# Kernel tuning notes

Hardware: AMD Instinct MI355X
Metric: run time of the kernel (lower is better)

## Reference

```python
import jax, jax.numpy as jnp
import numpy as np

N_NODES = 50000
N_EDGES = 800000
N_GRAPHS = 256
F_IN, HID, EMB = 128, 256, 128
N_GROUPS, N_FAM = 16, 128


def setup_inputs() -> dict:
    key = jax.random.key(0)
    ks = jax.random.split(key, 12)
    x = jax.random.normal(ks[0], (N_NODES, F_IN), dtype=jnp.float32)
    edge_index = jax.random.randint(ks[1], (2, N_EDGES), 0, N_NODES, dtype=jnp.int64)
    batch = jnp.sort(jax.random.randint(ks[2], (N_NODES,), 0, N_GRAPHS, dtype=jnp.int64))
    def lin(k, fi, fo):
        s = 1.0 / np.sqrt(fi)
        return jax.random.uniform(k, (fi, fo), minval=-s, maxval=s, dtype=jnp.float32)
    W1 = lin(ks[3], F_IN, HID); b1 = jnp.zeros((HID,), jnp.float32)
    W2 = lin(ks[4], HID, EMB); b2 = jnp.zeros((EMB,), jnp.float32)
    Wg = lin(ks[5], EMB, N_GROUPS); bg = jnp.zeros((N_GROUPS,), jnp.float32)
    s = 1.0 / np.sqrt(EMB)
    Wf = jax.random.uniform(ks[6], (N_GROUPS, EMB, N_FAM), minval=-s, maxval=s, dtype=jnp.float32)
    bf = jnp.zeros((N_GROUPS, N_FAM), jnp.float32)
    return {"x": x, "edge_index": edge_index, "batch": batch,
            "W1": W1, "b1": b1, "W2": W2, "b2": b2,
            "Wg": Wg, "bg": bg, "Wf": Wf, "bf": bf}


def _gcn_conv(h, src, dst, coef, W, b, n):
    # h: [N, Fin]; src/dst: [E'] (self-loops included); coef: [E'] sym-norm
    hw = h @ W                                    # [N, Fout]
    msg = hw[src] * coef[:, None]                 # gather + scale, [E', Fout]
    out = jax.ops.segment_sum(msg, dst, num_segments=n)  # scatter-add
    return out + b


def reference(x, edge_index, batch, W1, b1, W2, b2, Wg, bg, Wf, bf):
    n = x.shape[0]
    loops = jnp.arange(n, dtype=edge_index.dtype)
    src = jnp.concatenate([edge_index[0], loops])
    dst = jnp.concatenate([edge_index[1], loops])
    # symmetric GCN normalization (deg >= 1 thanks to self-loops)
    deg = jax.ops.segment_sum(jnp.ones_like(dst, dtype=x.dtype), dst, num_segments=n)
    dinv = jax.lax.rsqrt(deg)
    coef = dinv[src] * dinv[dst]

    h1 = jax.nn.relu(_gcn_conv(x, src, dst, coef, W1, b1, n))  # dropout = identity (eval)
    h2 = _gcn_conv(h1, src, dst, coef, W2, b2, n)

    # global mean pool over graphs
    sums = jax.ops.segment_sum(h2, batch, num_segments=N_GRAPHS)
    cnts = jax.ops.segment_sum(jnp.ones((n,), x.dtype), batch, num_segments=N_GRAPHS)
    embeddings = sums / jnp.maximum(cnts, 1.0)[:, None]        # [G, EMB]

    group_logits = embeddings @ Wg + bg                        # [G, n_groups]
    pred_groups = jnp.argmax(group_logits, axis=1)             # routing
    # per-graph routed family classifier (dense equivalent of the dict outputs)
    family_logits = jnp.einsum('gd,gdf->gf', embeddings, Wf[pred_groups]) + bf[pred_groups]
    return embeddings, group_logits, family_logits
```

## Files before the change

kernel.cpp:

```cpp
#include <hip/hip_runtime.h>
#include <hip/hip_fp16.h>
#include <cstddef>
#include <cstdint>

static constexpr int NN   = 50000;
static constexpr int NE   = 800000;
static constexpr int NG   = 256;
static constexpr int FIN  = 128;
static constexpr int HID  = 256;
static constexpr int EMB  = 128;
static constexpr int NGRP = 16;
static constexpr int NFAM = 128;
static constexpr int NETOT = NE + NN;

static constexpr int SCAN_B  = 256;
static constexpr int SCAN_CH = (NN + SCAN_B - 1) / SCAN_B;

static constexpr int NSLICE  = 8;
static constexpr int SLICE_W = (NN + NSLICE - 1) / NSLICE;
static constexpr int BUILD_RANKS = 64;

using bf16x8 = __attribute__((ext_vector_type(8))) short;
using f32x4  = __attribute__((ext_vector_type(4))) float;

__device__ __forceinline__ unsigned short f2bf(float f) {
    uint32_t u = __float_as_uint(f);
    u += 0x7FFFu + ((u >> 16) & 1u);
    return (unsigned short)(u >> 16);
}
__device__ __forceinline__ float bf2f(unsigned short u) {
    return __uint_as_float((uint32_t)u << 16);
}
__device__ __forceinline__ uint32_t pack_sw(int s, float w) {
    return (uint32_t)s | ((uint32_t)__half_as_ushort(__float2half(w)) << 16);
}
__device__ __forceinline__ void unpack_sw(uint32_t v, int& s, float& w) {
    s = (int)(v & 0xFFFFu);
    w = __half2float(__ushort_as_half((unsigned short)(v >> 16)));
}


__global__ void k_count(const int* __restrict__ edst, int* __restrict__ degi, int e) {
    int i = blockIdx.x * blockDim.x + threadIdx.x;
    if (i < e) atomicAdd(degi + edst[i], 1);
}

__global__ void k_prep(const int* __restrict__ degi, const int* __restrict__ batch,
                       float* __restrict__ dinv, int* __restrict__ gstart,
                       float* __restrict__ emb_acc, int n, int G) {
    int i = blockIdx.x * blockDim.x + threadIdx.x;
    if (i < NG * EMB) emb_acc[i] = 0.f;
    if (i >= n) return;
    dinv[i] = rsqrtf((float)(degi[i] + 1));
    int b  = batch[i];
    int pb = (i == 0) ? -1 : batch[i - 1];
    for (int g = pb + 1; g <= b; ++g) gstart[g] = i;
    if (i == n - 1) {
        for (int g = b + 1; g <= G; ++g) gstart[g] = n;
    }
}

__global__ void k_xconv(const float* __restrict__ x, const float* __restrict__ dinv,
                        unsigned short* __restrict__ xs) {
    int t = blockIdx.x * blockDim.x + threadIdx.x;
    size_t i = (size_t)t * 8;
    float dv = dinv[t >> 4];
    float4 a = *(const float4*)(x + i);
    float4 b = *(const float4*)(x + i + 4);
    uint4 o;
    o.x = (uint32_t)f2bf(dv * a.x) | ((uint32_t)f2bf(dv * a.y) << 16);
    o.y = (uint32_t)f2bf(dv * a.z) | ((uint32_t)f2bf(dv * a.w) << 16);
    o.z = (uint32_t)f2bf(dv * b.x) | ((uint32_t)f2bf(dv * b.y) << 16);
    o.w = (uint32_t)f2bf(dv * b.z) | ((uint32_t)f2bf(dv * b.w) << 16);
    *(uint4*)(xs + i) = o;
}

__global__ void k_wconv(const float* __restrict__ W1, const float* __restrict__ W2,
                        unsigned short* __restrict__ W1t, unsigned short* __restrict__ W2t) {
    int t = blockIdx.x * blockDim.x + threadIdx.x;
    if (t < HID * FIN) {
        int nidx = t >> 7, k = t & 127;
        W1t[t] = f2bf(W1[(size_t)k * HID + nidx]);
    } else {
        int u = t - HID * FIN;
        int nidx = u >> 8, k = u & 255;
        W2t[u] = f2bf(W2[(size_t)k * EMB + nidx]);
    }
}


__global__ __launch_bounds__(256) void k_scanA(const int* __restrict__ degi,
                                               int* __restrict__ row_ptr,
                                               int* __restrict__ bsum, int n) {
    __shared__ int sh[256];
    const int b = blockIdx.x, t = threadIdx.x;
    const int idx = b * SCAN_CH + t;
    int v = 0;
    if (t < SCAN_CH && idx < n) v = degi[idx] + 1;
    sh[t] = v;
    __syncthreads();
    for (int off = 1; off < 256; off <<= 1) {
        int y = (t >= off) ? sh[t - off] : 0;
        __syncthreads();
        if (t >= off) sh[t] += y;
        __syncthreads();
    }
    if (t < SCAN_CH && idx < n) row_ptr[idx] = sh[t] - v;
    if (t == 255) bsum[b] = sh[255];
}

__global__ __launch_bounds__(256) void k_scanB(const int* __restrict__ bsum,
                                               const int* __restrict__ gstart,
                                               float* __restrict__ rcnt,
                                               int* __restrict__ row_ptr,
                                               int* __restrict__ cursor, int n) {
    __shared__ int sh[SCAN_B];
    const int b = blockIdx.x, t = threadIdx.x;
    sh[t] = bsum[t];
    __syncthreads();
    for (int off = 1; off < SCAN_B; off <<= 1) {
        int y = (t >= off) ? sh[t - off] : 0;
        __syncthreads();
        if (t >= off) sh[t] += y;
        __syncthreads();
    }
    const int boff = (b == 0) ? 0 : sh[b - 1];
    const int idx  = b * SCAN_CH + t;
    if (t < SCAN_CH && idx < n) {
        row_ptr[idx] += boff;
        cursor[idx] = 1;
    }
    if (b == 0 && t == 0) row_ptr[n] = sh[SCAN_B - 1];
    if (b == 0 && t < NG) {
        int c = gstart[t + 1] - gstart[t];
        rcnt[t] = 1.0f / (float)max(c, 1);
    }
}


__global__ __launch_bounds__(256) void k_build(
        const int* __restrict__ esrc, const int* __restrict__ edst,
        const int* __restrict__ batch, const float* __restrict__ dinv,
        const float* __restrict__ rcnt, const int* __restrict__ row_ptr,
        int* __restrict__ cursor, uint32_t* __restrict__ eP, int n, int e) {
    const int slice = blockIdx.x & 7;
    const int rank  = blockIdx.x >> 3;
    const int lo = slice * SLICE_W;
    const int hi = min(lo + SLICE_W, n);
    for (int i = lo + rank * 256 + (int)threadIdx.x; i < hi; i += BUILD_RANKS * 256) {
        eP[row_ptr[i]] = pack_sw(i, dinv[i] * rcnt[batch[i]]);
    }
    for (int j = rank * 256 + (int)threadIdx.x; j < e; j += BUILD_RANKS * 256) {
        int d = edst[j];
        if (d < lo || d >= hi) continue;
        int s = esrc[j];
        int p = atomicAdd(cursor + d, 1);
        eP[row_ptr[d] + p] = pack_sw(s, dinv[d] * rcnt[batch[d]]);
    }
}


__global__ __launch_bounds__(256) void k_agg(
        const unsigned short* __restrict__ xs, const int* __restrict__ row_ptr,
        const uint32_t* __restrict__ eP, const float* __restrict__ dinv,
        unsigned short* __restrict__ xa, int n) {
    int node = blockIdx.x * 4 + (threadIdx.x >> 6);
    if (node >= n) return;
    int lane = threadIdx.x & 63;
    int grp = lane >> 4, fl = lane & 15;
    float acc[8] = {};
    int beg = row_ptr[node], end = row_ptr[node + 1];
    for (int j = beg; j < end; j += 4) {
        int jj = j + grp;
        bool valid = jj < end;
        uint32_t ev = __builtin_nontemporal_load(eP + (valid ? jj : beg));
        int s = (int)(ev & 0xFFFFu);
        float m = valid ? 1.f : 0.f;
        bf16x8 v = *(const bf16x8*)(xs + ((size_t)s << 7) + fl * 8);
#pragma unroll
        for (int k = 0; k < 8; ++k)
            acc[k] += m * bf2f((unsigned short)v[k]);
    }
#pragma unroll
    for (int k = 0; k < 8; ++k) {
        acc[k] += __shfl_xor(acc[k], 16);
        acc[k] += __shfl_xor(acc[k], 32);
    }
    if (lane < 16) {
        float di = dinv[node];
        uint4 o;
        o.x = (uint32_t)f2bf(di * acc[0]) | ((uint32_t)f2bf(di * acc[1]) << 16);
        o.y = (uint32_t)f2bf(di * acc[2]) | ((uint32_t)f2bf(di * acc[3]) << 16);
        o.z = (uint32_t)f2bf(di * acc[4]) | ((uint32_t)f2bf(di * acc[5]) << 16);
        o.w = (uint32_t)f2bf(di * acc[6]) | ((uint32_t)f2bf(di * acc[7]) << 16);
        *(uint4*)(xa + ((size_t)node << 7) + fl * 8) = o;
    }
}


__global__ __launch_bounds__(256) void k_fgemm(
        const unsigned short* __restrict__ A,
        const unsigned short* __restrict__ W1t,
        const unsigned short* __restrict__ W2t,
        const float* __restrict__ b1, const float* __restrict__ dinv,
        unsigned short* __restrict__ H, int M) {
    __shared__ unsigned short h1s[64 * 256];
    const int m0 = blockIdx.x * 64;
    const int w  = threadIdx.x >> 6;
    const int l  = threadIdx.x & 63;
    const int lr = l & 15;
    const int lk = l >> 4;

    {
        f32x4 acc[4][4] = {};
        const int n0 = w * 64;
#pragma unroll
        for (int ks = 0; ks < 4; ++ks) {
            const int k0 = ks * 32 + lk * 8;
            bf16x8 bfr[4];
#pragma unroll
            for (int ni = 0; ni < 4; ++ni)
                bfr[ni] = *(const bf16x8*)(W1t + (size_t)(n0 + ni * 16 + lr) * FIN + k0);
#pragma unroll
            for (int mi = 0; mi < 4; ++mi) {
                int row = min(m0 + mi * 16 + lr, M - 1);
                bf16x8 afr = *(const bf16x8*)(A + ((size_t)row << 7) + k0);
#pragma unroll
                for (int ni = 0; ni < 4; ++ni)
                    acc[mi][ni] = __builtin_amdgcn_mfma_f32_16x16x32_bf16(
                        afr, bfr[ni], acc[mi][ni], 0, 0, 0);
            }
        }
#pragma unroll
        for (int ni = 0; ni < 4; ++ni) {
            int col = n0 + ni * 16 + lr;
            float bb = b1[col];
#pragma unroll
            for (int mi = 0; mi < 4; ++mi) {
#pragma unroll
                for (int r = 0; r < 4; ++r) {
                    int rl = mi * 16 + lk * 4 + r;
                    float dv = dinv[min(m0 + rl, M - 1)];
                    float v = fmaxf(acc[mi][ni][r] + bb, 0.f) * dv;
                    int byte = (rl * 512 + col * 2) ^ ((rl & 7) << 4);
                    *(unsigned short*)((char*)h1s + byte) = f2bf(v);
                }
            }
        }
    }
    __syncthreads();
    f32x4 acc2[4][2] = {};
    {
        const int n0 = w * 32;
#pragma unroll
        for (int ks = 0; ks < 8; ++ks) {
            const int k0 = ks * 32 + lk * 8;
            bf16x8 bfr[2];
#pragma unroll
            for (int ni = 0; ni < 2; ++ni)
                bfr[ni] = *(const bf16x8*)(W2t + (size_t)(n0 + ni * 16 + lr) * HID + k0);
#pragma unroll
            for (int mi = 0; mi < 4; ++mi) {
                int rl = mi * 16 + lr;
                int byte = (rl * 512 + k0 * 2) ^ ((rl & 7) << 4);
                bf16x8 afr = *(const bf16x8*)((const char*)h1s + byte);
#pragma unroll
                for (int ni = 0; ni < 2; ++ni)
                    acc2[mi][ni] = __builtin_amdgcn_mfma_f32_16x16x32_bf16(
                        afr, bfr[ni], acc2[mi][ni], 0, 0, 0);
            }
        }
    }
    __syncthreads();
    {
        const int n0 = w * 32;
#pragma unroll
        for (int ni = 0; ni < 2; ++ni) {
            int col = n0 + ni * 16 + lr;
#pragma unroll
            for (int mi = 0; mi < 4; ++mi)
#pragma unroll
                for (int r = 0; r < 4; ++r) {
                    int rl = mi * 16 + lk * 4 + r;
                    h1s[rl * EMB + col] = f2bf(acc2[mi][ni][r]);
                }
        }
    }
    __syncthreads();
    int nrows = min(64, M - m0);
    for (int c = threadIdx.x; c < nrows * 16; c += 256) {
        int rl = c >> 4, cc = c & 15;
        *(uint4*)(H + ((size_t)(m0 + rl) << 7) + cc * 8) =
            *(const uint4*)(h1s + rl * EMB + cc * 8);
    }
}


__global__ __launch_bounds__(256) void k_pool(
        const unsigned short* __restrict__ H, const int* __restrict__ row_ptr,
        const int* __restrict__ gstart, const uint32_t* __restrict__ eP,
        float* __restrict__ emb_acc) {
    __shared__ float red[4][EMB];
    const int g  = blockIdx.x >> 3;
    const int kb = blockIdx.x & 7;
    const int e0 = row_ptr[gstart[g]];
    const int e1 = row_ptr[gstart[g + 1]];
    const int len = e1 - e0;
    const int per = (len + 7) >> 3;
    const int s0  = e0 + kb * per;
    const int s1  = min(s0 + per, e1);
    const int lane = threadIdx.x & 63;
    const int wv   = threadIdx.x >> 6;
    const int grp = lane >> 4, fl = lane & 15;

    float acc[8] = {};
    for (int j = s0 + wv * 4; j < s1; j += 16) {
        int jj = j + grp;
        bool valid = jj < s1;
        uint32_t ev = __builtin_nontemporal_load(eP + (valid ? jj : s0));
        int s; float wgt;
        unpack_sw(ev, s, wgt);
        if (!valid) wgt = 0.f;
        bf16x8 v = *(const bf16x8*)(H + ((size_t)s << 7) + fl * 8);
#pragma unroll
        for (int k = 0; k < 8; ++k)
            acc[k] += wgt * bf2f((unsigned short)v[k]);
    }
#pragma unroll
    for (int k = 0; k < 8; ++k) {
        acc[k] += __shfl_xor(acc[k], 16);
        acc[k] += __shfl_xor(acc[k], 32);
    }
    if (lane < 16) {
#pragma unroll
        for (int k = 0; k < 8; ++k) red[wv][fl * 8 + k] = acc[k];
    }
    __syncthreads();
    int t = threadIdx.x;
    if (t < EMB) {
        float v = red[0][t] + red[1][t] + red[2][t] + red[3][t];
        if (v != 0.f) atomicAdd(&emb_acc[g * EMB + t], v);
    }
}


__global__ __launch_bounds__(128) void k_head(const float* __restrict__ emb_acc,
                                              const int* __restrict__ gstart,
                                              const float* __restrict__ b2,
                                              const float* __restrict__ Wg,
                                              const float* __restrict__ bg,
                                              const float* __restrict__ Wf,
                                              const float* __restrict__ bff,
                                              float* __restrict__ out_emb,
                                              float* __restrict__ out_gl,
                                              float* __restrict__ out_fl) {
    __shared__ float e[EMB];
    __shared__ float gl[NGRP];
    __shared__ int ps;
    int g = blockIdx.x, c = threadIdx.x;
    bool nonempty = gstart[g + 1] > gstart[g];
    float a = emb_acc[g * EMB + c] + (nonempty ? b2[c] : 0.f);
    e[c] = a;
    out_emb[(size_t)g * EMB + c] = a;
    __syncthreads();
    if (c < NGRP) {
        float s = bg[c];
        for (int d = 0; d < EMB; ++d) s += e[d] * Wg[d * NGRP + c];
        gl[c] = s;
        out_gl[g * NGRP + c] = s;
    }
    __syncthreads();
    if (c == 0) {
        int bi = 0;
        float bv = gl[0];
        for (int t2 = 1; t2 < NGRP; ++t2)
            if (gl[t2] > bv) { bv = gl[t2]; bi = t2; }
        ps = bi;
    }
    __syncthreads();
    int pr = ps;
    float s = bff[pr * NFAM + c];
    for (int d = 0; d < EMB; ++d) s += e[d] * Wf[((size_t)pr * EMB + d) * NFAM + c];
    out_fl[g * NFAM + c] = s;
}


extern "C" void kernel_launch(void* const* d_in, const int* in_sizes, int n_in,
                              void* d_out, int out_size, void* d_ws, size_t ws_size,
                              hipStream_t stream) {
    const float* x   = (const float*)d_in[0];
    const int*   ei  = (const int*)d_in[1];
    const int*   bat = (const int*)d_in[2];
    const float* W1  = (const float*)d_in[3];
    const float* b1  = (const float*)d_in[4];
    const float* W2  = (const float*)d_in[5];
    const float* b2  = (const float*)d_in[6];
    const float* Wg  = (const float*)d_in[7];
    const float* bg  = (const float*)d_in[8];
    const float* Wf  = (const float*)d_in[9];
    const float* bf  = (const float*)d_in[10];

    float* out     = (float*)d_out;
    float* out_emb = out;
    float* out_gl  = out + (size_t)NG * EMB;
    float* out_fl  = out_gl + (size_t)NG * NGRP;

    char* w = (char*)d_ws;
    auto alloc = [&](size_t bytes) {
        char* p = w;
        w += (bytes + 255) & ~(size_t)255;
        return p;
    };
    int*            degi    = (int*)alloc((size_t)NN * 4);
    float*          dinv    = (float*)alloc((size_t)NN * 4);
    int*            row_ptr = (int*)alloc((size_t)(NN + 1) * 4);
    int*            cursor  = (int*)alloc((size_t)NN * 4);
    int*            bsum    = (int*)alloc((size_t)SCAN_B * 4);
    uint32_t*       eP      = (uint32_t*)alloc((size_t)NETOT * 4);
    int*            gstart  = (int*)alloc((size_t)(NG + 1) * 4);
    float*          rcnt    = (float*)alloc((size_t)NG * 4);
    unsigned short* xs      = (unsigned short*)alloc((size_t)NN * FIN * 2);
    unsigned short* xa      = (unsigned short*)alloc((size_t)NN * FIN * 2);
    unsigned short* W1t     = (unsigned short*)alloc((size_t)HID * FIN * 2);
    unsigned short* W2t     = (unsigned short*)alloc((size_t)EMB * HID * 2);
    unsigned short* H       = (unsigned short*)alloc((size_t)NN * EMB * 2);
    float*          emb_acc = (float*)alloc((size_t)NG * EMB * 4);

    const int* esrc = ei;
    const int* edst = ei + NE;

    hipMemsetAsync(degi, 0, (size_t)NN * 4, stream);
    k_count<<<(NE + 255) / 256, 256, 0, stream>>>(edst, degi, NE);
    k_prep<<<(NG * HID + 255) / 256, 256, 0, stream>>>(degi, bat, dinv, gstart,
                                                       emb_acc, NN, NG);
    k_xconv<<<(NN * 16) / 256, 256, 0, stream>>>(x, dinv, xs);
    k_wconv<<<(HID * FIN + EMB * HID) / 256, 256, 0, stream>>>(W1, W2, W1t, W2t);
    k_scanA<<<SCAN_B, 256, 0, stream>>>(degi, row_ptr, bsum, NN);
    k_scanB<<<SCAN_B, 256, 0, stream>>>(bsum, gstart, rcnt, row_ptr, cursor, NN);
    k_build<<<NSLICE * BUILD_RANKS, 256, 0, stream>>>(esrc, edst, bat, dinv, rcnt,
                                                      row_ptr, cursor, eP, NN, NE);

    k_agg<<<(NN + 3) / 4, 256, 0, stream>>>(xs, row_ptr, eP, dinv, xa, NN);
    k_fgemm<<<(NN + 63) / 64, 256, 0, stream>>>(xa, W1t, W2t, b1, dinv, H, NN);

    k_pool<<<NG * 8, 256, 0, stream>>>(H, row_ptr, gstart, eP, emb_acc);

    k_head<<<NG, 128, 0, stream>>>(emb_acc, gstart, b2, Wg, bg, Wf, bf,
                                   out_emb, out_gl, out_fl);
}
```

Measured before the change: 223.4 us.

## Pack CSR cursor and edge weight into one 64-bit word for single-pass build

The CSR build no longer uses 8 destination slices, each of which rescanned all edges. It now runs one thread per edge and does a single 64-bit atomicAdd on a combined word that holds the write cursor and the precomputed half-precision weight. The scanB kernel initialises this combined word and writes the self-loop entries, and the rcnt computation moves into scanA. This removes the repeated edge reads and the per-edge dinv, batch and rcnt lookups, at the cost of 64-bit atomics scattered over 50k destinations without slice locality.

```diff
diff --git a/kernel.cpp b/kernel.cpp
--- a/kernel.cpp
+++ b/kernel.cpp
@@ -16,10 +16,6 @@
 static constexpr int SCAN_B  = 256;
 static constexpr int SCAN_CH = (NN + SCAN_B - 1) / SCAN_B;
 
-static constexpr int NSLICE  = 8;
-static constexpr int SLICE_W = (NN + NSLICE - 1) / NSLICE;
-static constexpr int BUILD_RANKS = 64;
-
 using bf16x8 = __attribute__((ext_vector_type(8))) short;
 using f32x4  = __attribute__((ext_vector_type(4))) float;
 
@@ -30,9 +26,6 @@
 }
 __device__ __forceinline__ float bf2f(unsigned short u) {
     return __uint_as_float((uint32_t)u << 16);
-}
-__device__ __forceinline__ uint32_t pack_sw(int s, float w) {
-    return (uint32_t)s | ((uint32_t)__half_as_ushort(__float2half(w)) << 16);
 }
 __device__ __forceinline__ void unpack_sw(uint32_t v, int& s, float& w) {
     s = (int)(v & 0xFFFFu);
@@ -90,10 +83,16 @@
 
 
 __global__ __launch_bounds__(256) void k_scanA(const int* __restrict__ degi,
+                                               const int* __restrict__ gstart,
+                                               float* __restrict__ rcnt,
                                                int* __restrict__ row_ptr,
                                                int* __restrict__ bsum, int n) {
+    const int b = blockIdx.x, t = threadIdx.x;
+    if (b == 0 && t < NG) {
+        int c = gstart[t + 1] - gstart[t];
+        rcnt[t] = 1.0f / (float)max(c, 1);
+    }
     __shared__ int sh[256];
-    const int b = blockIdx.x, t = threadIdx.x;
     const int idx = b * SCAN_CH + t;
     int v = 0;
     if (t < SCAN_CH && idx < n) v = degi[idx] + 1;
@@ -110,10 +109,12 @@
 }
 
 __global__ __launch_bounds__(256) void k_scanB(const int* __restrict__ bsum,
-                                               const int* __restrict__ gstart,
-                                               float* __restrict__ rcnt,
+                                               const int* __restrict__ batch,
+                                               const float* __restrict__ dinv,
+                                               const float* __restrict__ rcnt,
                                                int* __restrict__ row_ptr,
-                                               int* __restrict__ cursor, int n) {
+                                               unsigned long long* __restrict__ combo,
+                                               uint32_t* __restrict__ eP, int n) {
     __shared__ int sh[SCAN_B];
     const int b = blockIdx.x, t = threadIdx.x;
     sh[t] = bsum[t];
@@ -127,36 +128,28 @@
     const int boff = (b == 0) ? 0 : sh[b - 1];
     const int idx  = b * SCAN_CH + t;
     if (t < SCAN_CH && idx < n) {
-        row_ptr[idx] += boff;
-        cursor[idx] = 1;
+        int rp = row_ptr[idx] + boff;
+        row_ptr[idx] = rp;
+        unsigned short wh = __half_as_ushort(
+            __float2half(dinv[idx] * rcnt[batch[idx]]));
+        combo[idx] = ((unsigned long long)wh << 32) | (unsigned int)(rp + 1);
+        eP[rp] = (uint32_t)idx | ((uint32_t)wh << 16);
     }
     if (b == 0 && t == 0) row_ptr[n] = sh[SCAN_B - 1];
-    if (b == 0 && t < NG) {
-        int c = gstart[t + 1] - gstart[t];
-        rcnt[t] = 1.0f / (float)max(c, 1);
-    }
-}
-
-
-__global__ __launch_bounds__(256) void k_build(
-        const int* __restrict__ esrc, const int* __restrict__ edst,
-        const int* __restrict__ batch, const float* __restrict__ dinv,
-        const float* __restrict__ rcnt, const int* __restrict__ row_ptr,
-        int* __restrict__ cursor, uint32_t* __restrict__ eP, int n, int e) {
-    const int slice = blockIdx.x & 7;
-    const int rank  = blockIdx.x >> 3;
-    const int lo = slice * SLICE_W;
-    const int hi = min(lo + SLICE_W, n);
-    for (int i = lo + rank * 256 + (int)threadIdx.x; i < hi; i += BUILD_RANKS * 256) {
-        eP[row_ptr[i]] = pack_sw(i, dinv[i] * rcnt[batch[i]]);
-    }
-    for (int j = rank * 256 + (int)threadIdx.x; j < e; j += BUILD_RANKS * 256) {
-        int d = edst[j];
-        if (d < lo || d >= hi) continue;
-        int s = esrc[j];
-        int p = atomicAdd(cursor + d, 1);
-        eP[row_ptr[d] + p] = pack_sw(s, dinv[d] * rcnt[batch[d]]);
-    }
+}
+
+
+__global__ void k_build(const int* __restrict__ esrc, const int* __restrict__ edst,
+                        unsigned long long* __restrict__ combo,
+                        uint32_t* __restrict__ eP, int e) {
+    int j = blockIdx.x * blockDim.x + threadIdx.x;
+    if (j >= e) return;
+    int d = edst[j];
+    int s = esrc[j];
+    unsigned long long old = atomicAdd(combo + d, 1ull);
+    uint32_t slot = (uint32_t)old;
+    uint32_t wh   = (uint32_t)(old >> 32) & 0xFFFFu;
+    eP[slot] = (uint32_t)s | (wh << 16);
 }
 
 
@@ -411,20 +404,20 @@
         w += (bytes + 255) & ~(size_t)255;
         return p;
     };
-    int*            degi    = (int*)alloc((size_t)NN * 4);
-    float*          dinv    = (float*)alloc((size_t)NN * 4);
-    int*            row_ptr = (int*)alloc((size_t)(NN + 1) * 4);
-    int*            cursor  = (int*)alloc((size_t)NN * 4);
-    int*            bsum    = (int*)alloc((size_t)SCAN_B * 4);
-    uint32_t*       eP      = (uint32_t*)alloc((size_t)NETOT * 4);
-    int*            gstart  = (int*)alloc((size_t)(NG + 1) * 4);
-    float*          rcnt    = (float*)alloc((size_t)NG * 4);
-    unsigned short* xs      = (unsigned short*)alloc((size_t)NN * FIN * 2);
-    unsigned short* xa      = (unsigned short*)alloc((size_t)NN * FIN * 2);
-    unsigned short* W1t     = (unsigned short*)alloc((size_t)HID * FIN * 2);
-    unsigned short* W2t     = (unsigned short*)alloc((size_t)EMB * HID * 2);
-    unsigned short* H       = (unsigned short*)alloc((size_t)NN * EMB * 2);
-    float*          emb_acc = (float*)alloc((size_t)NG * EMB * 4);
+    int*                 degi    = (int*)alloc((size_t)NN * 4);
+    float*               dinv    = (float*)alloc((size_t)NN * 4);
+    int*                 row_ptr = (int*)alloc((size_t)(NN + 1) * 4);
+    unsigned long long*  combo   = (unsigned long long*)alloc((size_t)NN * 8);
+    int*                 bsum    = (int*)alloc((size_t)SCAN_B * 4);
+    uint32_t*            eP      = (uint32_t*)alloc((size_t)NETOT * 4);
+    int*                 gstart  = (int*)alloc((size_t)(NG + 1) * 4);
+    float*               rcnt    = (float*)alloc((size_t)NG * 4);
+    unsigned short*      xs      = (unsigned short*)alloc((size_t)NN * FIN * 2);
+    unsigned short*      xa      = (unsigned short*)alloc((size_t)NN * FIN * 2);
+    unsigned short*      W1t     = (unsigned short*)alloc((size_t)HID * FIN * 2);
+    unsigned short*      W2t     = (unsigned short*)alloc((size_t)EMB * HID * 2);
+    unsigned short*      H       = (unsigned short*)alloc((size_t)NN * EMB * 2);
+    float*               emb_acc = (float*)alloc((size_t)NG * EMB * 4);
 
     const int* esrc = ei;
     const int* edst = ei + NE;
@@ -435,10 +428,9 @@
                                                        emb_acc, NN, NG);
     k_xconv<<<(NN * 16) / 256, 256, 0, stream>>>(x, dinv, xs);
     k_wconv<<<(HID * FIN + EMB * HID) / 256, 256, 0, stream>>>(W1, W2, W1t, W2t);
-    k_scanA<<<SCAN_B, 256, 0, stream>>>(degi, row_ptr, bsum, NN);
-    k_scanB<<<SCAN_B, 256, 0, stream>>>(bsum, gstart, rcnt, row_ptr, cursor, NN);
-    k_build<<<NSLICE * BUILD_RANKS, 256, 0, stream>>>(esrc, edst, bat, dinv, rcnt,
-                                                      row_ptr, cursor, eP, NN, NE);
+    k_scanA<<<SCAN_B, 256, 0, stream>>>(degi, gstart, rcnt, row_ptr, bsum, NN);
+    k_scanB<<<SCAN_B, 256, 0, stream>>>(bsum, bat, dinv, rcnt, row_ptr, combo, eP, NN);
+    k_build<<<(NE + 255) / 256, 256, 0, stream>>>(esrc, edst, combo, eP, NE);
 
     k_agg<<<(NN + 3) / 4, 256, 0, stream>>>(xs, row_ptr, eP, dinv, xa, NN);
     k_fgemm<<<(NN + 63) / 64, 256, 0, stream>>>(xa, W1t, W2t, b1, dinv, H, NN);
```

Result: no change. 226.7 us, median of 3 (+1.5%).
